# Optimization experiments

Hardware: AMD Instinct MI355X
Metric: run time of the kernel (lower is better)

## Reference

```python
import jax, jax.numpy as jnp
import numpy as np
from jax import lax

B, L, T = 200000, 64, 16  # symbols, input length (== filter_size), channel taps


def _conv1d(x, w, stride):
    # x: [N, Cin, L], w: [Cout, Cin, K] -> [N, Cout, Lout]; lax conv = correlation (matches torch)
    return lax.conv_general_dilated(x, w, (stride,), 'VALID',
                                    dimension_numbers=('NCH', 'OIH', 'NCH'))


def setup_inputs() -> dict:
    key = jax.random.key(0)
    ks = jax.random.split(key, 7)
    return {
        'x': jax.random.normal(ks[0], (B, 2, L), dtype=jnp.float32),
        'conv1_w': jax.random.normal(ks[1], (1, 2, L // 4), dtype=jnp.float32) * 0.1,
        'conv1_b': jax.random.normal(ks[2], (1,), dtype=jnp.float32) * 0.1,
        'conv2_w': jax.random.normal(ks[3], (2, 1, 4), dtype=jnp.float32) * 0.1,
        'conv2_b': jax.random.normal(ks[4], (2,), dtype=jnp.float32) * 0.1,
        'taps_real': jax.random.normal(ks[5], (T,), dtype=jnp.float32),
        'taps_imag': jax.random.normal(ks[6], (T,), dtype=jnp.float32),
    }


def reference(x, conv1_w, conv1_b, conv2_w, conv2_b, taps_real, taps_imag):
    k1 = conv1_w.shape[2]  # filter_size // 4; stride == kernel
    h = jax.nn.elu(_conv1d(x, conv1_w, k1) + conv1_b[None, :, None])   # [B,1,4]
    rst = jax.nn.elu(_conv1d(h, conv2_w, 1) + conv2_b[None, :, None])  # [B,2,1]

    nT = taps_real.shape[0]
    sr = rst[:, 0, 0]  # real sequence over the batch/time axis, [B]
    si = rst[:, 1, 0]
    pr = jnp.pad(sr, (nT - 1, 0))  # causal zero padding, as torch.cat(zeros, rst)
    pi = jnp.pad(si, (nT - 1, 0))
    # torch code correlates windows with flipped taps -> use flipped taps as corr kernel
    hr = jnp.flip(taps_real)
    hi = jnp.flip(taps_imag)

    def corr(sig, ker):
        return lax.conv_general_dilated(sig[None, None, :], ker[None, None, :], (1,),
                                        'VALID', dimension_numbers=('NCH', 'OIH', 'NCH'))[0, 0]

    y_real = corr(pr, hr) - corr(pi, hi)  # [B]
    y_imag = corr(pr, hi) + corr(pi, hr)
    return jnp.stack([y_real, y_imag], axis=1)[:, :, None]  # [B,2,1]
```

## Files before the change

kernel.cpp:

```cpp
#include <hip/hip_runtime.h>
#include <math.h>

#define BLOCK 256
#define EPB 64
#define TAPS 16
#define HALO (TAPS - 1)

__device__ __forceinline__ float eluf(float v) { return v > 0.0f ? v : expm1f(v); }
__device__ __forceinline__ float dot4(float4 a, float4 b) {
    return a.x * b.x + a.y * b.y + a.z * b.z + a.w * b.w;
}

__global__ __launch_bounds__(BLOCK, 4) void NF_conv_kernel(
    const float* __restrict__ x,
    const float* __restrict__ w1, const float* __restrict__ b1,
    const float* __restrict__ w2, const float* __restrict__ b2,
    float2* __restrict__ s, int B)
{
    __shared__ float4 xs[EPB * 32];

    const int t = threadIdx.x;
    const int b0 = blockIdx.x * EPB;
    const float4* xf4 = reinterpret_cast<const float4*>(x);
    const float4* w1v = reinterpret_cast<const float4*>(w1);

    float4 tmp[8];
    const long gbase = (long)b0 * 32;
    const bool full = (b0 + EPB) <= B;
    if (full) {
#pragma unroll
        for (int k = 0; k < 8; ++k)
            tmp[k] = xf4[gbase + k * 256 + t];
    } else {
#pragma unroll
        for (int k = 0; k < 8; ++k) {
            int e = 8 * k + (t >> 5);
            tmp[k] = (b0 + e < B) ? xf4[gbase + k * 256 + t]
                                  : make_float4(0.f, 0.f, 0.f, 0.f);
        }
    }
#pragma unroll
    for (int k = 0; k < 8; ++k) {
        int e = 8 * k + (t >> 5);
        int i = t & 31;
        xs[e * 32 + (i ^ (e & 7))] = tmp[k];
    }
    __syncthreads();

    const int e = t >> 2;
    const int j = t & 3;
    float acc = b1[0];
#pragma unroll
    for (int c = 0; c < 2; ++c)
#pragma unroll
        for (int p = 0; p < 4; ++p)
            acc += dot4(xs[e * 32 + ((c * 16 + j * 4 + p) ^ (e & 7))], w1v[c * 4 + p]);
    float h = eluf(acc);

    float pr = h * w2[j];
    float pi = h * w2[4 + j];
    pr += __shfl_xor(pr, 1);  pr += __shfl_xor(pr, 2);
    pi += __shfl_xor(pi, 1);  pi += __shfl_xor(pi, 2);

    if (j == 0 && (b0 + e) < B) {
        float sr = eluf(pr + b2[0]);
        float si = eluf(pi + b2[1]);
        s[b0 + e] = make_float2(sr, si);
    }
}

__global__ __launch_bounds__(BLOCK) void NF_fir_kernel(
    const float2* __restrict__ s,
    const float* __restrict__ tr, const float* __restrict__ ti,
    float2* __restrict__ out, int B)
{
    __shared__ float s_r[BLOCK + HALO];
    __shared__ float s_i[BLOCK + HALO];

    const int t = threadIdx.x;
    const long base = (long)blockIdx.x * BLOCK;
    const long b = base + t;

    if (t < HALO) {
        long hb = base - HALO + t;
        float2 v = (hb >= 0) ? s[hb] : make_float2(0.f, 0.f);
        s_r[t] = v.x;  s_i[t] = v.y;
    }
    {
        float2 v = (b < B) ? s[b] : make_float2(0.f, 0.f);
        s_r[HALO + t] = v.x;  s_i[HALO + t] = v.y;
    }
    __syncthreads();

    if (b < B) {
        float yr = 0.f, yi = 0.f;
#pragma unroll
        for (int jj = 0; jj < TAPS; ++jj) {
            float a = s_r[HALO + t - jj];
            float c = s_i[HALO + t - jj];
            float trj = tr[jj], tij = ti[jj];
            yr += a * trj - c * tij;
            yi += a * tij + c * trj;
        }
        out[b] = make_float2(yr, yi);
    }
}

extern "C" void kernel_launch(void* const* d_in, const int* in_sizes, int n_in,
                              void* d_out, int out_size, void* d_ws, size_t ws_size,
                              hipStream_t stream) {
    const float* x  = (const float*)d_in[0];
    const float* w1 = (const float*)d_in[1];
    const float* b1 = (const float*)d_in[2];
    const float* w2 = (const float*)d_in[3];
    const float* b2 = (const float*)d_in[4];
    const float* tr = (const float*)d_in[5];
    const float* ti = (const float*)d_in[6];
    float2* out = (float2*)d_out;

    const int B = in_sizes[0] / 128;
    float2* s = (float2*)d_ws;

    const int grid1 = (B + EPB - 1) / EPB;
    NF_conv_kernel<<<grid1, BLOCK, 0, stream>>>(x, w1, b1, w2, b2, s, B);

    const int grid2 = (B + BLOCK - 1) / BLOCK;
    NF_fir_kernel<<<grid2, BLOCK, 0, stream>>>(s, tr, ti, out, B);
}
```

Before: 25.30 us.

## Fuse conv and FIR stages into one kernel with recomputed halo

Merges the conv stage and the FIR stage into a single kernel. Each block computes 256 conv outputs into shared memory and recomputes the 15-element causal halo from x instead of reading it from a workspace buffer. The x loads move from a coalesced shared-memory staging to direct strided float4 reads, with four lanes per element reduced by shuffles. This removes one launch and the workspace round trip. In exchange it adds redundant halo compute, uses 1024-thread blocks, and leaves only a quarter of the threads active in the FIR phase.

```diff
diff --git a/kernel.cpp b/kernel.cpp
--- a/kernel.cpp
+++ b/kernel.cpp
@@ -1,108 +1,97 @@
 #include <hip/hip_runtime.h>
 #include <math.h>
 
-#define BLOCK 256
-#define EPB 64
+#define BLOCK 1024
+#define EPB 256
 #define TAPS 16
-#define HALO (TAPS - 1)
+#define HWIN 16
 
-__device__ __forceinline__ float eluf(float v) { return v > 0.0f ? v : expm1f(v); }
+__device__ __forceinline__ float eluf(float v) { return v > 0.f ? v : expm1f(v); }
 __device__ __forceinline__ float dot4(float4 a, float4 b) {
     return a.x * b.x + a.y * b.y + a.z * b.z + a.w * b.w;
 }
 
-__global__ __launch_bounds__(BLOCK, 4) void NF_conv_kernel(
+__device__ __forceinline__ void conv_elem(const float4* __restrict__ xf4, long ge,
+        int j, float4 wv0, float4 wv1, float b1s,
+        const float* __restrict__ w2, float b20, float b21,
+        float& sr, float& si)
+{
+    const float4* base = xf4 + ge * 32;
+    float4 v[8];
+#pragma unroll
+    for (int p = 0; p < 8; ++p) v[p] = base[4 * p + j];
+
+    float a0 = 0.f, a1 = 0.f, a2 = 0.f, a3 = 0.f;
+    a0 += dot4(v[0], wv0); a1 += dot4(v[1], wv0); a2 += dot4(v[2], wv0); a3 += dot4(v[3], wv0);
+    a0 += dot4(v[4], wv1); a1 += dot4(v[5], wv1); a2 += dot4(v[6], wv1); a3 += dot4(v[7], wv1);
+
+    a0 += __shfl_xor(a0, 1); a1 += __shfl_xor(a1, 1);
+    a2 += __shfl_xor(a2, 1); a3 += __shfl_xor(a3, 1);
+    a0 += __shfl_xor(a0, 2); a1 += __shfl_xor(a1, 2);
+    a2 += __shfl_xor(a2, 2); a3 += __shfl_xor(a3, 2);
+
+    float h0 = eluf(a0 + b1s), h1 = eluf(a1 + b1s);
+    float h2 = eluf(a2 + b1s), h3 = eluf(a3 + b1s);
+
+    float pr = b20 + h0 * w2[0] + h1 * w2[1] + h2 * w2[2] + h3 * w2[3];
+    float pi = b21 + h0 * w2[4] + h1 * w2[5] + h2 * w2[6] + h3 * w2[7];
+    sr = eluf(pr);
+    si = eluf(pi);
+}
+
+__global__ __launch_bounds__(BLOCK, 4) void NF_20581483282566_kernel(
     const float* __restrict__ x,
     const float* __restrict__ w1, const float* __restrict__ b1,
     const float* __restrict__ w2, const float* __restrict__ b2,
-    float2* __restrict__ s, int B)
+    const float* __restrict__ tr, const float* __restrict__ ti,
+    float2* __restrict__ out, int B)
 {
-    __shared__ float4 xs[EPB * 32];
+    __shared__ float s_r[HWIN + EPB];
+    __shared__ float s_i[HWIN + EPB];
 
     const int t = threadIdx.x;
-    const int b0 = blockIdx.x * EPB;
+    const int j = t & 3;
+    const int e_loc = t >> 2;
+    const long b0 = (long)blockIdx.x * EPB;
+    const long ge = b0 + e_loc;
+
     const float4* xf4 = reinterpret_cast<const float4*>(x);
     const float4* w1v = reinterpret_cast<const float4*>(w1);
+    const float4 wv0 = w1v[j];
+    const float4 wv1 = w1v[4 + j];
+    const float b1s = b1[0];
+    const float b20 = b2[0], b21 = b2[1];
 
-    float4 tmp[8];
-    const long gbase = (long)b0 * 32;
-    const bool full = (b0 + EPB) <= B;
-    if (full) {
-#pragma unroll
-        for (int k = 0; k < 8; ++k)
-            tmp[k] = xf4[gbase + k * 256 + t];
-    } else {
-#pragma unroll
-        for (int k = 0; k < 8; ++k) {
-            int e = 8 * k + (t >> 5);
-            tmp[k] = (b0 + e < B) ? xf4[gbase + k * 256 + t]
-                                  : make_float4(0.f, 0.f, 0.f, 0.f);
-        }
+    if (ge < B) {
+        float sr, si;
+        conv_elem(xf4, ge, j, wv0, wv1, b1s, w2, b20, b21, sr, si);
+        if (j == 0) { s_r[HWIN + e_loc] = sr; s_i[HWIN + e_loc] = si; }
     }
-#pragma unroll
-    for (int k = 0; k < 8; ++k) {
-        int e = 8 * k + (t >> 5);
-        int i = t & 31;
-        xs[e * 32 + (i ^ (e & 7))] = tmp[k];
+
+    if (t < 4 * HWIN) {
+        const int eh = t >> 2;
+        const long he = b0 - HWIN + eh;
+        float sr = 0.f, si = 0.f;
+        if (he >= 0)
+            conv_elem(xf4, he, j, wv0, wv1, b1s, w2, b20, b21, sr, si);
+        if (j == 0) { s_r[eh] = sr; s_i[eh] = si; }
     }
     __syncthreads();
 
-    const int e = t >> 2;
-    const int j = t & 3;
-    float acc = b1[0];
+    if (t < EPB) {
+        const long b = b0 + t;
+        if (b < B) {
+            float yr = 0.f, yi = 0.f;
 #pragma unroll
-    for (int c = 0; c < 2; ++c)
-#pragma unroll
-        for (int p = 0; p < 4; ++p)
-            acc += dot4(xs[e * 32 + ((c * 16 + j * 4 + p) ^ (e & 7))], w1v[c * 4 + p]);
-    float h = eluf(acc);
-
-    float pr = h * w2[j];
-    float pi = h * w2[4 + j];
-    pr += __shfl_xor(pr, 1);  pr += __shfl_xor(pr, 2);
-    pi += __shfl_xor(pi, 1);  pi += __shfl_xor(pi, 2);
-
-    if (j == 0 && (b0 + e) < B) {
-        float sr = eluf(pr + b2[0]);
-        float si = eluf(pi + b2[1]);
-        s[b0 + e] = make_float2(sr, si);
-    }
-}
-
-__global__ __launch_bounds__(BLOCK) void NF_fir_kernel(
-    const float2* __restrict__ s,
-    const float* __restrict__ tr, const float* __restrict__ ti,
-    float2* __restrict__ out, int B)
-{
-    __shared__ float s_r[BLOCK + HALO];
-    __shared__ float s_i[BLOCK + HALO];
-
-    const int t = threadIdx.x;
-    const long base = (long)blockIdx.x * BLOCK;
-    const long b = base + t;
-
-    if (t < HALO) {
-        long hb = base - HALO + t;
-        float2 v = (hb >= 0) ? s[hb] : make_float2(0.f, 0.f);
-        s_r[t] = v.x;  s_i[t] = v.y;
-    }
-    {
-        float2 v = (b < B) ? s[b] : make_float2(0.f, 0.f);
-        s_r[HALO + t] = v.x;  s_i[HALO + t] = v.y;
-    }
-    __syncthreads();
-
-    if (b < B) {
-        float yr = 0.f, yi = 0.f;
-#pragma unroll
-        for (int jj = 0; jj < TAPS; ++jj) {
-            float a = s_r[HALO + t - jj];
-            float c = s_i[HALO + t - jj];
-            float trj = tr[jj], tij = ti[jj];
-            yr += a * trj - c * tij;
-            yi += a * tij + c * trj;
+            for (int jj = 0; jj < TAPS; ++jj) {
+                float a = s_r[HWIN + t - jj];
+                float c = s_i[HWIN + t - jj];
+                float trj = tr[jj], tij = ti[jj];
+                yr += a * trj - c * tij;
+                yi += a * tij + c * trj;
+            }
+            out[b] = make_float2(yr, yi);
         }
-        out[b] = make_float2(yr, yi);
     }
 }
 
@@ -119,11 +108,6 @@
     float2* out = (float2*)d_out;
 
     const int B = in_sizes[0] / 128;
-    float2* s = (float2*)d_ws;
-
-    const int grid1 = (B + EPB - 1) / EPB;
-    NF_conv_kernel<<<grid1, BLOCK, 0, stream>>>(x, w1, b1, w2, b2, s, B);
-
-    const int grid2 = (B + BLOCK - 1) / BLOCK;
-    NF_fir_kernel<<<grid2, BLOCK, 0, stream>>>(s, tr, ti, out, B);
+    const int grid = (B + EPB - 1) / EPB;
+    NF_20581483282566_kernel<<<grid, BLOCK, 0, stream>>>(x, w1, b1, w2, b2, tr, ti, out, B);
 }
```

Result: faster. 24.03 us (-5.0%).
